# Performance work log

Hardware: AMD Instinct MI355X
Metric: run time of the kernel (lower is better)

The kernel has to match this reference:

```python
import jax, jax.numpy as jnp
import numpy as np

B = 1024      # batch of seed nodes
S = 16        # sample_size
H = 256       # hidden
IN = 150      # in_dim + NUM_CLASS (128 + 22)
OUT = 22
HEADS = 8
NN = 100000   # number of graph nodes
LN_EPS = 1e-5


def setup_inputs() -> dict:
    key = jax.random.key(0)
    ks = jax.random.split(key, 16)
    sc = 0.05
    return {
        "node_feats": jax.random.normal(ks[0], (NN, IN), jnp.float32),
        "batch": jax.random.randint(ks[1], (B,), 0, NN),
        "nbr2": jax.random.randint(ks[2], (B, S), 0, NN),
        "nbr1": jax.random.randint(ks[3], (B * (S + 1), S), 0, NN),
        "W_in": jax.random.normal(ks[4], (IN, H), jnp.float32) * sc,
        "b_in": jnp.zeros((H,), jnp.float32),
        "Wqkv": jax.random.normal(ks[5], (2, 3, H, H), jnp.float32) * sc,
        "bqkv": jnp.zeros((2, 3, H), jnp.float32),
        "Wo": jax.random.normal(ks[6], (2, H, H), jnp.float32) * sc,
        "bo": jnp.zeros((2, H), jnp.float32),
        "Wf": jax.random.normal(ks[7], (2, H, H), jnp.float32) * sc,
        "bf": jnp.zeros((2, H), jnp.float32),
        "ln_g": jnp.ones((4, H), jnp.float32),
        "ln_b": jnp.zeros((4, H), jnp.float32),
        "W_out": jax.random.normal(ks[8], (H, OUT), jnp.float32) * sc,
        "b_out": jnp.zeros((OUT,), jnp.float32),
    }


def _layer_norm(x, g, b):
    m = jnp.mean(x, axis=-1, keepdims=True)
    v = jnp.mean((x - m) ** 2, axis=-1, keepdims=True)
    return (x - m) * jax.lax.rsqrt(v + LN_EPS) * g + b


def _mha(q, kv, Wq, Wk, Wv, bq, bk, bv, Wout, bout):
    # q: [N, 1, H], kv: [N, S, H]; single-query multi-head attention
    N, Sk, _ = kv.shape
    dh = H // HEADS
    qp = (q @ Wq + bq).reshape(N, 1, HEADS, dh)
    kp = (kv @ Wk + bk).reshape(N, Sk, HEADS, dh)
    vp = (kv @ Wv + bv).reshape(N, Sk, HEADS, dh)
    att = jax.nn.softmax(
        jnp.einsum("nqhd,nkhd->nhqk", qp, kp) / np.float32(np.sqrt(dh)), axis=-1
    )
    o = jnp.einsum("nhqk,nkhd->nqhd", att, vp).reshape(N, 1, H)
    return o @ Wout + bout


def _attn_block(x, l, Wqkv, bqkv, Wo, bo, Wf, bf, ln_g, ln_b):
    # x: [N, S+1, H]; slot 0 is the query (self), rest are sampled neighbors
    q, kv = x[:, 0:1, :], x[:, 1:, :]
    h = _mha(q, kv, Wqkv[l, 0], Wqkv[l, 1], Wqkv[l, 2],
             bqkv[l, 0], bqkv[l, 1], bqkv[l, 2], Wo[l], bo[l])
    h = h[:, 0, :] + q[:, 0, :]                       # residual
    h = _layer_norm(h, ln_g[2 * l], ln_b[2 * l])
    h = h + (h @ Wf[l] + bf[l])                       # FFN (single Linear) + residual
    return _layer_norm(h, ln_g[2 * l + 1], ln_b[2 * l + 1])


def reference(node_feats, batch, nbr2, nbr1, W_in, b_in, Wqkv, bqkv, Wo, bo,
              Wf, bf, ln_g, ln_b, W_out, b_out):
    # Recursive neighbor expansion (unrolled for layers=2)
    ids1 = jnp.concatenate([batch[:, None], nbr2], axis=1).reshape(-1)   # [B*(S+1)]
    ids0 = jnp.concatenate([ids1[:, None], nbr1], axis=1).reshape(-1)    # [B*(S+1)^2]
    # layer 0: proj_in(features) = ReLU(Linear) (Dropout identity in eval)
    h0 = jax.nn.relu(node_feats[ids0] @ W_in + b_in)                     # [M0, H]
    # layer 1
    h1 = _attn_block(h0.reshape(B * (S + 1), S + 1, H), 0,
                     Wqkv, bqkv, Wo, bo, Wf, bf, ln_g, ln_b)
    # layer 2
    h2 = _attn_block(h1.reshape(B, S + 1, H), 1,
                     Wqkv, bqkv, Wo, bo, Wf, bf, ln_g, ln_b)
    # proj_out: Linear -> Softmax
    return jax.nn.softmax(h2 @ W_out + b_out, axis=-1)
```

## Files before the change

kernel.cpp:

```cpp
#include <hip/hip_runtime.h>
#include <hip/hip_bf16.h>
#include <math.h>

typedef unsigned short ushort_t;
typedef __bf16 bf16x8 __attribute__((ext_vector_type(8)));
typedef float  f32x4  __attribute__((ext_vector_type(4)));
typedef __attribute__((address_space(1))) const unsigned int* gas_t;
typedef __attribute__((address_space(3))) unsigned int* las_t;

#define B_SZ   1024
#define SEQ    17
#define KVN    16
#define HDIM   256
#define NHEAD  8
#define DH     32
#define INF    150
#define OUTD   22
#define LN_EPS 1e-5f
#define N1     (B_SZ * SEQ)
#define NN_    100000
#define NKVBLK 1563
#define NHQBLK 272

constexpr size_t SZ_H0    = (size_t)NN_ * 256 * 2;
constexpr size_t SZ_KV0   = (size_t)NN_ * 512 * 2;
constexpr size_t SZ_ROW   = (size_t)N1 * 256 * 2;
constexpr size_t OFF_HQ   = 0;
constexpr size_t OFF_KV0  = OFF_HQ + SZ_H0;
constexpr size_t OFF_QKV1 = OFF_KV0;
constexpr size_t OFF_O1   = OFF_QKV1 + (size_t)N1 * 768 * 2;
constexpr size_t OFF_H2   = OFF_O1 + (size_t)B_SZ * 256 * 2;
constexpr size_t OFF_Q0   = OFF_KV0 + SZ_KV0;
constexpr size_t OFF_O0   = OFF_Q0 + SZ_ROW;
constexpr size_t OFF_H1   = OFF_O0;
constexpr size_t OFF_IDS  = OFF_O0 + SZ_ROW;
constexpr size_t OFF_WTIN = OFF_IDS + (size_t)N1 * 4;
constexpr size_t OFF_WKV0 = OFF_WTIN + 256 * 160 * 2;
constexpr size_t OFF_WQ0  = OFF_WKV0 + 512 * 256 * 2;
constexpr size_t OFF_WKVQ1= OFF_WQ0 + 256 * 256 * 2;
constexpr size_t OFF_WO0  = OFF_WKVQ1 + 768 * 256 * 2;
constexpr size_t OFF_WF0  = OFF_WO0 + 256 * 256 * 2;
constexpr size_t OFF_WO1  = OFF_WF0 + 256 * 256 * 2;
constexpr size_t OFF_WF1  = OFF_WO1 + 256 * 256 * 2;
constexpr size_t OFF_B1   = OFF_WF1 + 256 * 256 * 2;

__device__ __forceinline__ ushort_t f2bfu(float x) {
    __hip_bfloat16 h = __float2bfloat16(x);
    return *reinterpret_cast<ushort_t*>(&h);
}
__device__ __forceinline__ float bfu2f(ushort_t u) {
    __hip_bfloat16 h;
    *reinterpret_cast<ushort_t*>(&h) = u;
    return __bfloat162float(h);
}
__device__ __forceinline__ f32x4 mfma16(bf16x8 a, bf16x8 b, f32x4 c) {
    return __builtin_amdgcn_mfma_f32_16x16x32_bf16(a, b, c, 0, 0, 0);
}

__device__ __forceinline__ void stage_b(
    const ushort_t* __restrict__ Bsrc, int Kld, int kk,
    ushort_t* lbase, int w, int lane) {
    #pragma unroll
    for (int i = 0; i < 4; ++i) {
        int inst = w * 4 + i;
        int row = inst * 16 + (lane >> 2);
        int q_log = (lane & 3) ^ ((row >> 1) & 3);
        const ushort_t* src = Bsrc + (size_t)row * Kld + kk + q_log * 8;
        __builtin_amdgcn_global_load_lds((gas_t)(const void*)src,
                                         (las_t)(void*)(lbase + inst * 512),
                                         16, 0, 0);
    }
}

__global__ __launch_bounds__(256) void k_prep(
    const float* __restrict__ W_in, const float* __restrict__ Wqkv,
    const float* __restrict__ Wo, const float* __restrict__ Wf,
    const float* __restrict__ bqkv,
    const int* __restrict__ batch, const int* __restrict__ nbr2,
    char* __restrict__ ws) {
    const int job = blockIdx.y;
    const int idx = blockIdx.x * 256 + threadIdx.x;
    if (job == 11) {
        if (idx < N1) {
            int b = idx / SEQ, s = idx % SEQ;
            ((int*)(ws + OFF_IDS))[idx] = (s == 0) ? batch[b] : nbr2[b * KVN + s - 1];
        }
        return;
    }
    if (job == 12) {
        if (idx < 768) ((float*)(ws + OFF_B1))[idx] = bqkv[768 + ((idx + 256) % 768)];
        return;
    }
    const float* src = nullptr; ushort_t* dst = nullptr;
    int Kpad = 256, Kvalid = 256;
    switch (job) {
        case 0:  src = W_in;           dst = (ushort_t*)(ws + OFF_WTIN); Kpad = 160; Kvalid = 150; break;
        case 1:  src = Wqkv + 65536;   dst = (ushort_t*)(ws + OFF_WKV0); break;
        case 2:  src = Wqkv + 131072;  dst = (ushort_t*)(ws + OFF_WKV0) + 65536; break;
        case 3:  src = Wqkv;           dst = (ushort_t*)(ws + OFF_WQ0); break;
        case 4:  src = Wqkv + 262144;  dst = (ushort_t*)(ws + OFF_WKVQ1); break;
        case 5:  src = Wqkv + 327680;  dst = (ushort_t*)(ws + OFF_WKVQ1) + 65536; break;
        case 6:  src = Wqkv + 196608;  dst = (ushort_t*)(ws + OFF_WKVQ1) + 131072; break;
        case 7:  src = Wo;             dst = (ushort_t*)(ws + OFF_WO0); break;
        case 8:  src = Wo + 65536;     dst = (ushort_t*)(ws + OFF_WO1); break;
        case 9:  src = Wf;             dst = (ushort_t*)(ws + OFF_WF0); break;
        case 10: src = Wf + 65536;     dst = (ushort_t*)(ws + OFF_WF1); break;
    }
    const int total = 256 * Kpad;
    if (idx >= total) return;
    int n = idx / Kpad, k = idx % Kpad;
    dst[idx] = (k < Kvalid) ? f2bfu(src[(size_t)k * 256 + n]) : (ushort_t)0;
}

__global__ __launch_bounds__(256) void k_fused(
    const float* __restrict__ nf,
    const ushort_t* __restrict__ Wt_in, const float* __restrict__ b_in,
    const ushort_t* __restrict__ Wkv, const ushort_t* __restrict__ Wq,
    const float* __restrict__ bqkv, const int* __restrict__ ids1,
    ushort_t* __restrict__ kv0, ushort_t* __restrict__ hq,
    ushort_t* __restrict__ q0) {
    __shared__ ushort_t Ah[64 * 256];
    __shared__ ushort_t Bbuf[2 * 8192];
    const int tid = threadIdx.x;
    const bool iskv = blockIdx.x < NKVBLK;
    const int m0 = (iskv ? blockIdx.x : blockIdx.x - NKVBLK) * 64;
    const int lane = tid & 63, w = tid >> 6;
    const int lr = lane & 15, q4 = lane >> 4, lk = q4 * 8;

    {
        ushort_t (*Astage)[168] = reinterpret_cast<ushort_t (*)[168]>(Ah);
        #pragma unroll
        for (int i = 0; i < 5; ++i) {
            int flat = tid + i * 256;
            int row = flat / 20, ch = flat % 20;
            int gm; 
            if (iskv) { gm = m0 + row; if (gm >= NN_) gm = 0; }
            else      { gm = ids1[m0 + row]; }
            const float* ap = nf + (size_t)gm * INF + ch * 8;
            ushort_t tmp[8];
            if (ch < 18) {
                #pragma unroll
                for (int j = 0; j < 4; ++j) {
                    float2 f = *reinterpret_cast<const float2*>(ap + j * 2);
                    tmp[j * 2] = f2bfu(f.x); tmp[j * 2 + 1] = f2bfu(f.y);
                }
            } else {
                #pragma unroll
                for (int j = 0; j < 8; ++j) {
                    int k = ch * 8 + j;
                    tmp[j] = (k < INF) ? f2bfu(ap[j]) : (ushort_t)0;
                }
            }
            *reinterpret_cast<int4*>(&Astage[row][ch * 8]) = *reinterpret_cast<int4*>(tmp);
        }
    }
    stage_b(Wt_in, 160, 0, Bbuf, w, lane);
    __syncthreads();

    f32x4 acc1[4][4] = {};
    {
        ushort_t (*Astage)[168] = reinterpret_cast<ushort_t (*)[168]>(Ah);
        for (int s = 0; s < 5; ++s) {
            const int cur = s & 1;
            if (s < 4) stage_b(Wt_in, 160, (s + 1) * 32, Bbuf + (cur ^ 1) * 8192, w, lane);
            bf16x8 a[4], b[4];
            #pragma unroll
            for (int mi = 0; mi < 4; ++mi)
                a[mi] = *reinterpret_cast<const bf16x8*>(&Astage[mi * 16 + lr][s * 32 + lk]);
            #pragma unroll
            for (int ni = 0; ni < 4; ++ni) {
                int n = w * 64 + ni * 16 + lr;
                b[ni] = *reinterpret_cast<const bf16x8*>(
                    &Bbuf[cur * 8192 + n * 32 + ((q4 ^ ((n >> 1) & 3)) * 8)]);
            }
            #pragma unroll
            for (int mi = 0; mi < 4; ++mi)
                #pragma unroll
                for (int ni = 0; ni < 4; ++ni)
                    acc1[mi][ni] = mfma16(a[mi], b[ni], acc1[mi][ni]);
            __syncthreads();
        }
    }

    #pragma unroll
    for (int ni = 0; ni < 4; ++ni) {
        int col = w * 64 + ni * 16 + lr;
        float bb = b_in[col];
        #pragma unroll
        for (int mi = 0; mi < 4; ++mi)
            #pragma unroll
            for (int r = 0; r < 4; ++r) {
                int row = mi * 16 + q4 * 4 + r;
                Ah[row * 256 + (col ^ ((row & 7) << 3))] =
                    f2bfu(fmaxf(acc1[mi][ni][r] + bb, 0.f));
            }
    }
    __syncthreads();

    if (!iskv) {
        #pragma unroll
        for (int i = 0; i < 8; ++i) {
            int flat = tid + i * 256;
            int row = flat >> 5, ch = flat & 31;
            *reinterpret_cast<int4*>(hq + (size_t)(m0 + row) * 256 + ch * 8) =
                *reinterpret_cast<const int4*>(&Ah[row * 256 + ((ch ^ (row & 7)) * 8)]);
        }
    }

    const int npass = iskv ? 2 : 1;
    for (int h = 0; h < npass; ++h) {
        const ushort_t* Bm = iskv ? (Wkv + (size_t)h * 65536) : Wq;
        const float* bias = iskv ? (bqkv + 256 + h * 256) : bqkv;
        __syncthreads();
        stage_b(Bm, 256, 0, Bbuf, w, lane);
        __syncthreads();
        f32x4 acc2[4][4] = {};
        for (int s = 0; s < 8; ++s) {
            const int cur = s & 1;
            if (s < 7) stage_b(Bm, 256, (s + 1) * 32, Bbuf + (cur ^ 1) * 8192, w, lane);
            bf16x8 a[4], b[4];
            #pragma unroll
            for (int mi = 0; mi < 4; ++mi) {
                int row = mi * 16 + lr;
                int chunk = (s * 4 + q4) ^ (row & 7);
                a[mi] = *reinterpret_cast<const bf16x8*>(&Ah[row * 256 + chunk * 8]);
            }
            #pragma unroll
            for (int ni = 0; ni < 4; ++ni) {
                int n = w * 64 + ni * 16 + lr;
                b[ni] = *reinterpret_cast<const bf16x8*>(
                    &Bbuf[cur * 8192 + n * 32 + ((q4 ^ ((n >> 1) & 3)) * 8)]);
            }
            #pragma unroll
            for (int mi = 0; mi < 4; ++mi)
                #pragma unroll
                for (int ni = 0; ni < 4; ++ni)
                    acc2[mi][ni] = mfma16(a[mi], b[ni], acc2[mi][ni]);
            __syncthreads();
        }
        float bl[4];
        #pragma unroll
        for (int ni = 0; ni < 4; ++ni) bl[ni] = bias[w * 64 + ni * 16 + lr];
        ushort_t* outp = iskv ? kv0 : q0;
        const int ldo = iskv ? 512 : 256;
        const int coff = (iskv ? h * 256 : 0) + w * 64;
        ushort_t* Shw = Bbuf + w * 32 * 72;
        #pragma unroll
        for (int part = 0; part < 2; ++part) {
            #pragma unroll
            for (int mi2 = 0; mi2 < 2; ++mi2) {
                int mi = part * 2 + mi2;
                #pragma unroll
                for (int ni = 0; ni < 4; ++ni)
                    #pragma unroll
                    for (int r = 0; r < 4; ++r)
                        Shw[(mi2 * 16 + q4 * 4 + r) * 72 + ni * 16 + lr] =
                            f2bfu(acc2[mi][ni][r] + bl[ni]);
            }
            #pragma unroll
            for (int j = 0; j < 4; ++j) {
                int flat = lane + j * 64;
                int r32 = flat >> 3, ch = flat & 7;
                int grow = m0 + part * 32 + r32;
                if (!iskv || grow < NN_)
                    *reinterpret_cast<int4*>(outp + (size_t)grow * ldo + coff + ch * 8) =
                        *reinterpret_cast<const int4*>(&Shw[r32 * 72 + ch * 8]);
            }
        }
    }
}

__global__ __launch_bounds__(256) void k_ffn(
    const ushort_t* __restrict__ Ain, const ushort_t* __restrict__ W1t,
    const float* __restrict__ b1,
    const ushort_t* __restrict__ resmat, int rstride,
    const float* __restrict__ lng1, const float* __restrict__ lnb1,
    const ushort_t* __restrict__ W2t, const float* __restrict__ b2,
    const float* __restrict__ lng2, const float* __restrict__ lnb2,
    ushort_t* __restrict__ out) {
    __shared__ ushort_t Al[32][264];
    __shared__ float xr[32][260];
    __shared__ float mrow[32], rrow[32];
    const int tid = threadIdx.x;
    const int m0 = blockIdx.x * 32;
    const int lane = tid & 63, w = tid >> 6;
    const int lr = lane & 15, q4 = lane >> 4, lk = q4 * 8;

    #pragma unroll
    for (int j = 0; j < 4; ++j) {
        int flat = tid + j * 256;
        int row = flat >> 5, ch = flat & 31;
        *reinterpret_cast<int4*>(&Al[row][ch * 8]) =
            *reinterpret_cast<const int4*>(Ain + (size_t)(m0 + row) * 256 + ch * 8);
    }
    __syncthreads();

    f32x4 acc[2][4];
    #pragma unroll
    for (int g = 0; g < 2; ++g) {
        const ushort_t* Wt = g ? W2t : W1t;
        #pragma unroll
        for (int mi = 0; mi < 2; ++mi)
            #pragma unroll
            for (int ni = 0; ni < 4; ++ni) acc[mi][ni] = f32x4{0.f, 0.f, 0.f, 0.f};
        bf16x8 bc[4];
        #pragma unroll
        for (int ni = 0; ni < 4; ++ni)
            bc[ni] = *reinterpret_cast<const bf16x8*>(
                Wt + (size_t)(w * 64 + ni * 16 + lr) * 256 + lk);
        #pragma unroll
        for (int s = 0; s < 8; ++s) {
            bf16x8 bn[4];
            if (s < 7) {
                #pragma unroll
                for (int ni = 0; ni < 4; ++ni)
                    bn[ni] = *reinterpret_cast<const bf16x8*>(
                        Wt + (size_t)(w * 64 + ni * 16 + lr) * 256 + (s + 1) * 32 + lk);
            }
            bf16x8 a0 = *reinterpret_cast<const bf16x8*>(&Al[lr][s * 32 + lk]);
            bf16x8 a1 = *reinterpret_cast<const bf16x8*>(&Al[16 + lr][s * 32 + lk]);
            #pragma unroll
            for (int ni = 0; ni < 4; ++ni) {
                acc[0][ni] = mfma16(a0, bc[ni], acc[0][ni]);
                acc[1][ni] = mfma16(a1, bc[ni], acc[1][ni]);
            }
            if (s < 7) {
                #pragma unroll
                for (int ni = 0; ni < 4; ++ni) bc[ni] = bn[ni];
            }
        }
        #pragma unroll
        for (int mi = 0; mi < 2; ++mi)
            #pragma unroll
            for (int ni = 0; ni < 4; ++ni)
                #pragma unroll
                for (int r = 0; r < 4; ++r)
                    xr[mi * 16 + q4 * 4 + r][w * 64 + ni * 16 + lr] = acc[mi][ni][r];
        __syncthreads();
        {
            float bb = g ? b2[tid] : b1[tid];
            if (g == 0) {
                for (int r = 0; r < 32; ++r)
                    xr[r][tid] += bb + bfu2f(resmat[(size_t)(m0 + r) * rstride * 256 + tid]);
            } else {
                for (int r = 0; r < 32; ++r)
                    xr[r][tid] += bb + bfu2f(Al[r][tid]);
            }
        }
        __syncthreads();
        for (int rr = w * 8; rr < w * 8 + 8; ++rr) {
            float4 v = *reinterpret_cast<const float4*>(&xr[rr][lane * 4]);
            float s1 = v.x + v.y + v.z + v.w;
            float s2 = v.x * v.x + v.y * v.y + v.z * v.z + v.w * v.w;
            #pragma unroll
            for (int off = 32; off > 0; off >>= 1) {
                s1 += __shfl_xor(s1, off);
                s2 += __shfl_xor(s2, off);
            }
            if (lane == 0) {
                float m = s1 * (1.f / 256.f);
                float var = s2 * (1.f / 256.f) - m * m;
                mrow[rr] = m;
                rrow[rr] = rsqrtf(var + LN_EPS);
            }
        }
        __syncthreads();
        if (g == 0) {
            float gg = lng1[tid], bb = lnb1[tid];
            for (int r = 0; r < 32; ++r)
                Al[r][tid] = f2bfu((xr[r][tid] - mrow[r]) * rrow[r] * gg + bb);
        } else {
            float gg = lng2[tid], bb = lnb2[tid];
            for (int r = 0; r < 32; ++r)
                out[(size_t)(m0 + r) * 256 + tid] =
                    f2bfu((xr[r][tid] - mrow[r]) * rrow[r] * gg + bb);
        }
        __syncthreads();
    }
}

__global__ __launch_bounds__(256) void k_qkv1(
    const ushort_t* __restrict__ h1, const ushort_t* __restrict__ Wt,
    const float* __restrict__ bias, ushort_t* __restrict__ outm) {
    __shared__ ushort_t Ah[64 * 256];
    __shared__ ushort_t Sh[4][32][72];
    const int tid = threadIdx.x;
    const int m0 = blockIdx.x * 64;
    const int lane = tid & 63, w = tid >> 6;
    const int lr = lane & 15, q4 = lane >> 4, lk = q4 * 8;

    #pragma unroll
    for (int i = 0; i < 8; ++i) {
        int flat = tid + i * 256;
        int row = flat >> 5, ch = flat & 31;
        *reinterpret_cast<int4*>(&Ah[row * 256 + ((ch ^ (row & 7)) * 8)]) =
            *reinterpret_cast<const int4*>(h1 + (size_t)(m0 + row) * 256 + ch * 8);
    }
    __syncthreads();

    for (int p = 0; p < 3; ++p) {
        f32x4 acc[4][4] = {};
        bf16x8 bc[4];
        #pragma unroll
        for (int ni = 0; ni < 4; ++ni)
            bc[ni] = *reinterpret_cast<const bf16x8*>(
                Wt + (size_t)(p * 256 + w * 64 + ni * 16 + lr) * 256 + lk);
        #pragma unroll
        for (int s = 0; s < 8; ++s) {
            bf16x8 bn[4];
            if (s < 7) {
                #pragma unroll
                for (int ni = 0; ni < 4; ++ni)
                    bn[ni] = *reinterpret_cast<const bf16x8*>(
                        Wt + (size_t)(p * 256 + w * 64 + ni * 16 + lr) * 256 + (s + 1) * 32 + lk);
            }
            bf16x8 a[4];
            #pragma unroll
            for (int mi = 0; mi < 4; ++mi) {
                int row = mi * 16 + lr;
                int chunk = (s * 4 + q4) ^ (row & 7);
                a[mi] = *reinterpret_cast<const bf16x8*>(&Ah[row * 256 + chunk * 8]);
            }
            #pragma unroll
            for (int mi = 0; mi < 4; ++mi)
                #pragma unroll
                for (int ni = 0; ni < 4; ++ni)
                    acc[mi][ni] = mfma16(a[mi], bc[ni], acc[mi][ni]);
            if (s < 7) {
                #pragma unroll
                for (int ni = 0; ni < 4; ++ni) bc[ni] = bn[ni];
            }
        }
        float bl[4];
        #pragma unroll
        for (int ni = 0; ni < 4; ++ni) bl[ni] = bias[p * 256 + w * 64 + ni * 16 + lr];
        const int coff = p * 256 + w * 64;
        #pragma unroll
        for (int part = 0; part < 2; ++part) {
            #pragma unroll
            for (int mi2 = 0; mi2 < 2; ++mi2) {
                int mi = part * 2 + mi2;
                #pragma unroll
                for (int ni = 0; ni < 4; ++ni)
                    #pragma unroll
                    for (int r = 0; r < 4; ++r)
                        Sh[w][mi2 * 16 + q4 * 4 + r][ni * 16 + lr] =
                            f2bfu(acc[mi][ni][r] + bl[ni]);
            }
            #pragma unroll
            for (int j = 0; j < 4; ++j) {
                int flat = lane + j * 64;
                int r32 = flat >> 3, ch = flat & 7;
                int grow = m0 + part * 32 + r32;
                *reinterpret_cast<int4*>(outm + (size_t)grow * 768 + coff + ch * 8) =
                    *reinterpret_cast<const int4*>(&Sh[w][r32][ch * 8]);
            }
        }
    }
}

__global__ __launch_bounds__(256) void attn_wave(
    const ushort_t* __restrict__ q_all, int qld, int qoff, int qstride,
    const ushort_t* __restrict__ kv_all, int kvld, int koff, int voff,
    const int* __restrict__ kvidx, int ngroups, ushort_t* __restrict__ o_out) {
    __shared__ ushort_t KL[4][KVN][264];
    __shared__ ushort_t VL[4][KVN][264];
    const int w = threadIdx.x >> 6, lane = threadIdx.x & 63;
    const int g = blockIdx.x * 4 + w;
    if (g >= ngroups) return;

    int idx16 = 0;
    if (lane < KVN)
        idx16 = kvidx ? kvidx[g * KVN + lane] : g * SEQ + 1 + lane;

    float qv[4];
    {
        uint2 u = *reinterpret_cast<const uint2*>(
            q_all + (size_t)g * qstride * qld + qoff + lane * 4);
        qv[0] = bfu2f((ushort_t)(u.x & 0xffff));
        qv[1] = bfu2f((ushort_t)(u.x >> 16));
        qv[2] = bfu2f((ushort_t)(u.y & 0xffff));
        qv[3] = bfu2f((ushort_t)(u.y >> 16));
    }
    {
        const int r = lane & 15, qtr = lane >> 4;
        int rid = __shfl(idx16, r);
        const ushort_t* kb = kv_all + (size_t)rid * kvld + koff;
        const ushort_t* vb = kv_all + (size_t)rid * kvld + voff;
        #pragma unroll
        for (int j = 0; j < 8; ++j) {
            int c8 = (qtr * 8 + j) * 8;
            *reinterpret_cast<int4*>(&KL[w][r][c8]) = *reinterpret_cast<const int4*>(kb + c8);
            *reinterpret_cast<int4*>(&VL[w][r][c8]) = *reinterpret_cast<const int4*>(vb + c8);
        }
    }
    float att[KVN];
    #pragma unroll
    for (int k = 0; k < KVN; ++k) {
        uint2 u = *reinterpret_cast<const uint2*>(&KL[w][k][lane * 4]);
        float p = qv[0] * bfu2f((ushort_t)(u.x & 0xffff))
                + qv[1] * bfu2f((ushort_t)(u.x >> 16))
                + qv[2] * bfu2f((ushort_t)(u.y & 0xffff))
                + qv[3] * bfu2f((ushort_t)(u.y >> 16));
        p += __shfl_xor(p, 1);
        p += __shfl_xor(p, 2);
        p += __shfl_xor(p, 4);
        att[k] = p * 0.17677669529663687f;
    }
    float m = att[0];
    #pragma unroll
    for (int k = 1; k < KVN; ++k) m = fmaxf(m, att[k]);
    float sum = 0.f;
    #pragma unroll
    for (int k = 0; k < KVN; ++k) { att[k] = __expf(att[k] - m); sum += att[k]; }
    float inv = 1.f / sum;
    float o[4] = {0.f, 0.f, 0.f, 0.f};
    #pragma unroll
    for (int k = 0; k < KVN; ++k) {
        uint2 u = *reinterpret_cast<const uint2*>(&VL[w][k][lane * 4]);
        float a = att[k] * inv;
        o[0] += a * bfu2f((ushort_t)(u.x & 0xffff));
        o[1] += a * bfu2f((ushort_t)(u.x >> 16));
        o[2] += a * bfu2f((ushort_t)(u.y & 0xffff));
        o[3] += a * bfu2f((ushort_t)(u.y >> 16));
    }
    uint2 r;
    r.x = (unsigned)f2bfu(o[0]) | ((unsigned)f2bfu(o[1]) << 16);
    r.y = (unsigned)f2bfu(o[2]) | ((unsigned)f2bfu(o[3]) << 16);
    *reinterpret_cast<uint2*>(o_out + (size_t)g * 256 + lane * 4) = r;
}

__global__ __launch_bounds__(64) void k_out(
    const ushort_t* __restrict__ h2, const float* __restrict__ W_out,
    const float* __restrict__ b_out, float* __restrict__ out) {
    const int b = blockIdx.x, j = threadIdx.x;
    __shared__ float xr[HDIM];
    for (int k = j; k < HDIM; k += 64) xr[k] = bfu2f(h2[(size_t)b * HDIM + k]);
    __syncthreads();
    float logit = -1e30f;
    if (j < OUTD) {
        float acc = b_out[j];
        for (int k = 0; k < HDIM; ++k) acc += xr[k] * W_out[k * OUTD + j];
        logit = acc;
    }
    float m = logit;
    #pragma unroll
    for (int off = 32; off > 0; off >>= 1) m = fmaxf(m, __shfl_xor(m, off));
    float e = (j < OUTD) ? __expf(logit - m) : 0.f;
    float s = e;
    #pragma unroll
    for (int off = 32; off > 0; off >>= 1) s += __shfl_xor(s, off);
    if (j < OUTD) out[(size_t)b * OUTD + j] = e / s;
}

extern "C" void kernel_launch(void* const* d_in, const int* in_sizes, int n_in,
                              void* d_out, int out_size, void* d_ws, size_t ws_size,
                              hipStream_t stream) {
    const float* nf    = (const float*)d_in[0];
    const int*   batch = (const int*)d_in[1];
    const int*   nbr2  = (const int*)d_in[2];
    const int*   nbr1  = (const int*)d_in[3];
    const float* W_in  = (const float*)d_in[4];
    const float* b_in  = (const float*)d_in[5];
    const float* Wqkv  = (const float*)d_in[6];
    const float* bqkv  = (const float*)d_in[7];
    const float* Wo    = (const float*)d_in[8];
    const float* bo    = (const float*)d_in[9];
    const float* Wf    = (const float*)d_in[10];
    const float* bf    = (const float*)d_in[11];
    const float* ln_g  = (const float*)d_in[12];
    const float* ln_b  = (const float*)d_in[13];
    const float* W_out = (const float*)d_in[14];
    const float* b_out = (const float*)d_in[15];
    float* out = (float*)d_out;
    char* ws = (char*)d_ws;

    ushort_t* hq   = (ushort_t*)(ws + OFF_HQ);
    ushort_t* kv0  = (ushort_t*)(ws + OFF_KV0);
    ushort_t* q0   = (ushort_t*)(ws + OFF_Q0);
    ushort_t* o0   = (ushort_t*)(ws + OFF_O0);
    ushort_t* h1   = (ushort_t*)(ws + OFF_H1);
    ushort_t* qkv1 = (ushort_t*)(ws + OFF_QKV1);
    ushort_t* o1   = (ushort_t*)(ws + OFF_O1);
    ushort_t* h2   = (ushort_t*)(ws + OFF_H2);
    const int* ids1 = (const int*)(ws + OFF_IDS);

    hipLaunchKernelGGL(k_prep, dim3(256, 13), dim3(256), 0, stream,
                       W_in, Wqkv, Wo, Wf, bqkv, batch, nbr2, ws);
    hipLaunchKernelGGL(k_fused, dim3(NKVBLK + NHQBLK), dim3(256), 0, stream,
                       nf, (const ushort_t*)(ws + OFF_WTIN), b_in,
                       (const ushort_t*)(ws + OFF_WKV0),
                       (const ushort_t*)(ws + OFF_WQ0), bqkv, ids1,
                       kv0, hq, q0);
    hipLaunchKernelGGL(attn_wave, dim3(N1 / 4), dim3(256), 0, stream,
                       q0, 256, 0, 1, kv0, 512, 0, 256, nbr1, N1, o0);
    hipLaunchKernelGGL(k_ffn, dim3(N1 / 32), dim3(256), 0, stream,
                       o0, (const ushort_t*)(ws + OFF_WO0), bo,
                       hq, 1, ln_g, ln_b,
                       (const ushort_t*)(ws + OFF_WF0), bf,
                       ln_g + 256, ln_b + 256, h1);
    hipLaunchKernelGGL(k_qkv1, dim3(N1 / 64), dim3(256), 0, stream,
                       h1, (const ushort_t*)(ws + OFF_WKVQ1),
                       (const float*)(ws + OFF_B1), qkv1);
    hipLaunchKernelGGL(attn_wave, dim3(B_SZ / 4), dim3(256), 0, stream,
                       qkv1, 768, 512, 17, qkv1, 768, 0, 256,
                       (const int*)nullptr, B_SZ, o1);
    hipLaunchKernelGGL(k_ffn, dim3(B_SZ / 32), dim3(256), 0, stream,
                       o1, (const ushort_t*)(ws + OFF_WO1), bo + 256,
                       h1, 17, ln_g + 512, ln_b + 512,
                       (const ushort_t*)(ws + OFF_WF1), bf + 256,
                       ln_g + 768, ln_b + 768, h2);
    hipLaunchKernelGGL(k_out, dim3(B_SZ), dim3(64), 0, stream,
                       h2, W_out, b_out, out);
}
```

Before: 275.8 us.

## Enlarge fused projection tile to 128 rows with 512-thread blocks

The fused input-projection and KV/Q-projection kernel now processes 128 rows per block with 8 waves in a 2x4 grid instead of 64 rows with 4 waves. Each staged weight tile is reused across twice as many rows, which halves weight traffic per output row. Double-buffered weight staging is replaced by a single buffer with barriers around each stage, so load latency is no longer hidden behind compute. The epilogue drops the LDS-staged coalesced 16-byte stores and writes scalar bf16 values straight to global memory, which may cost store efficiency. Shared memory per block grows to about 80KB, which limits how many blocks fit on a CU.

After: 306.6 us. +11.2%, slower.

```diff
diff --git a/kernel.cpp b/kernel.cpp
--- a/kernel.cpp
+++ b/kernel.cpp
@@ -19,8 +19,8 @@
 #define LN_EPS 1e-5f
 #define N1     (B_SZ * SEQ)
 #define NN_    100000
-#define NKVBLK 1563
-#define NHQBLK 272
+#define NKV2   782
+#define NHQ2   136
 
 constexpr size_t SZ_H0    = (size_t)NN_ * 256 * 2;
 constexpr size_t SZ_KV0   = (size_t)NN_ * 512 * 2;
@@ -57,12 +57,12 @@
     return __builtin_amdgcn_mfma_f32_16x16x32_bf16(a, b, c, 0, 0, 0);
 }
 
-__device__ __forceinline__ void stage_b(
+__device__ __forceinline__ void stage_b512(
     const ushort_t* __restrict__ Bsrc, int Kld, int kk,
     ushort_t* lbase, int w, int lane) {
     #pragma unroll
-    for (int i = 0; i < 4; ++i) {
-        int inst = w * 4 + i;
+    for (int i = 0; i < 2; ++i) {
+        int inst = w * 2 + i;
         int row = inst * 16 + (lane >> 2);
         int q_log = (lane & 3) ^ ((row >> 1) & 3);
         const ushort_t* src = Bsrc + (size_t)row * Kld + kk + q_log * 8;
@@ -112,28 +112,29 @@
     dst[idx] = (k < Kvalid) ? f2bfu(src[(size_t)k * 256 + n]) : (ushort_t)0;
 }
 
-__global__ __launch_bounds__(256) void k_fused(
+__global__ __launch_bounds__(512, 4) void k_fused(
     const float* __restrict__ nf,
     const ushort_t* __restrict__ Wt_in, const float* __restrict__ b_in,
     const ushort_t* __restrict__ Wkv, const ushort_t* __restrict__ Wq,
     const float* __restrict__ bqkv, const int* __restrict__ ids1,
     ushort_t* __restrict__ kv0, ushort_t* __restrict__ hq,
     ushort_t* __restrict__ q0) {
-    __shared__ ushort_t Ah[64 * 256];
-    __shared__ ushort_t Bbuf[2 * 8192];
+    __shared__ ushort_t Ah[128 * 256];
+    __shared__ ushort_t Bst[8192];
     const int tid = threadIdx.x;
-    const bool iskv = blockIdx.x < NKVBLK;
-    const int m0 = (iskv ? blockIdx.x : blockIdx.x - NKVBLK) * 64;
+    const bool iskv = blockIdx.x < NKV2;
+    const int m0 = (iskv ? blockIdx.x : blockIdx.x - NKV2) * 128;
     const int lane = tid & 63, w = tid >> 6;
+    const int wr = w >> 2, wc = w & 3;
     const int lr = lane & 15, q4 = lane >> 4, lk = q4 * 8;
 
     {
         ushort_t (*Astage)[168] = reinterpret_cast<ushort_t (*)[168]>(Ah);
         #pragma unroll
         for (int i = 0; i < 5; ++i) {
-            int flat = tid + i * 256;
+            int flat = tid + i * 512;
             int row = flat / 20, ch = flat % 20;
-            int gm; 
+            int gm;
             if (iskv) { gm = m0 + row; if (gm >= NN_) gm = 0; }
             else      { gm = ids1[m0 + row]; }
             const float* ap = nf + (size_t)gm * INF + ch * 8;
@@ -154,43 +155,44 @@
             *reinterpret_cast<int4*>(&Astage[row][ch * 8]) = *reinterpret_cast<int4*>(tmp);
         }
     }
-    stage_b(Wt_in, 160, 0, Bbuf, w, lane);
     __syncthreads();
 
     f32x4 acc1[4][4] = {};
     {
         ushort_t (*Astage)[168] = reinterpret_cast<ushort_t (*)[168]>(Ah);
         for (int s = 0; s < 5; ++s) {
-            const int cur = s & 1;
-            if (s < 4) stage_b(Wt_in, 160, (s + 1) * 32, Bbuf + (cur ^ 1) * 8192, w, lane);
+            __builtin_amdgcn_s_barrier();
+            stage_b512(Wt_in, 160, s * 32, Bst, w, lane);
+            __syncthreads();
             bf16x8 a[4], b[4];
             #pragma unroll
             for (int mi = 0; mi < 4; ++mi)
-                a[mi] = *reinterpret_cast<const bf16x8*>(&Astage[mi * 16 + lr][s * 32 + lk]);
+                a[mi] = *reinterpret_cast<const bf16x8*>(
+                    &Astage[wr * 64 + mi * 16 + lr][s * 32 + lk]);
             #pragma unroll
             for (int ni = 0; ni < 4; ++ni) {
-                int n = w * 64 + ni * 16 + lr;
+                int n = wc * 64 + ni * 16 + lr;
                 b[ni] = *reinterpret_cast<const bf16x8*>(
-                    &Bbuf[cur * 8192 + n * 32 + ((q4 ^ ((n >> 1) & 3)) * 8)]);
+                    &Bst[n * 32 + ((q4 ^ ((n >> 1) & 3)) * 8)]);
             }
             #pragma unroll
             for (int mi = 0; mi < 4; ++mi)
                 #pragma unroll
                 for (int ni = 0; ni < 4; ++ni)
                     acc1[mi][ni] = mfma16(a[mi], b[ni], acc1[mi][ni]);
-            __syncthreads();
-        }
-    }
+        }
+    }
+    __syncthreads();
 
     #pragma unroll
     for (int ni = 0; ni < 4; ++ni) {
-        int col = w * 64 + ni * 16 + lr;
+        int col = wc * 64 + ni * 16 + lr;
         float bb = b_in[col];
         #pragma unroll
         for (int mi = 0; mi < 4; ++mi)
             #pragma unroll
             for (int r = 0; r < 4; ++r) {
-                int row = mi * 16 + q4 * 4 + r;
+                int row = wr * 64 + mi * 16 + q4 * 4 + r;
                 Ah[row * 256 + (col ^ ((row & 7) << 3))] =
                     f2bfu(fmaxf(acc1[mi][ni][r] + bb, 0.f));
             }
@@ -200,7 +202,7 @@
     if (!iskv) {
         #pragma unroll
         for (int i = 0; i < 8; ++i) {
-            int flat = tid + i * 256;
+            int flat = tid + i * 512;
             int row = flat >> 5, ch = flat & 31;
             *reinterpret_cast<int4*>(hq + (size_t)(m0 + row) * 256 + ch * 8) =
                 *reinterpret_cast<const int4*>(&Ah[row * 256 + ((ch ^ (row & 7)) * 8)]);
@@ -211,61 +213,45 @@
     for (int h = 0; h < npass; ++h) {
         const ushort_t* Bm = iskv ? (Wkv + (size_t)h * 65536) : Wq;
         const float* bias = iskv ? (bqkv + 256 + h * 256) : bqkv;
-        __syncthreads();
-        stage_b(Bm, 256, 0, Bbuf, w, lane);
-        __syncthreads();
         f32x4 acc2[4][4] = {};
         for (int s = 0; s < 8; ++s) {
-            const int cur = s & 1;
-            if (s < 7) stage_b(Bm, 256, (s + 1) * 32, Bbuf + (cur ^ 1) * 8192, w, lane);
+            __builtin_amdgcn_s_barrier();
+            stage_b512(Bm, 256, s * 32, Bst, w, lane);
+            __syncthreads();
             bf16x8 a[4], b[4];
             #pragma unroll
             for (int mi = 0; mi < 4; ++mi) {
-                int row = mi * 16 + lr;
+                int row = wr * 64 + mi * 16 + lr;
                 int chunk = (s * 4 + q4) ^ (row & 7);
                 a[mi] = *reinterpret_cast<const bf16x8*>(&Ah[row * 256 + chunk * 8]);
             }
             #pragma unroll
             for (int ni = 0; ni < 4; ++ni) {
-                int n = w * 64 + ni * 16 + lr;
+                int n = wc * 64 + ni * 16 + lr;
                 b[ni] = *reinterpret_cast<const bf16x8*>(
-                    &Bbuf[cur * 8192 + n * 32 + ((q4 ^ ((n >> 1) & 3)) * 8)]);
+                    &Bst[n * 32 + ((q4 ^ ((n >> 1) & 3)) * 8)]);
             }
             #pragma unroll
             for (int mi = 0; mi < 4; ++mi)
                 #pragma unroll
                 for (int ni = 0; ni < 4; ++ni)
                     acc2[mi][ni] = mfma16(a[mi], b[ni], acc2[mi][ni]);
-            __syncthreads();
-        }
-        float bl[4];
-        #pragma unroll
-        for (int ni = 0; ni < 4; ++ni) bl[ni] = bias[w * 64 + ni * 16 + lr];
+        }
         ushort_t* outp = iskv ? kv0 : q0;
         const int ldo = iskv ? 512 : 256;
-        const int coff = (iskv ? h * 256 : 0) + w * 64;
-        ushort_t* Shw = Bbuf + w * 32 * 72;
-        #pragma unroll
-        for (int part = 0; part < 2; ++part) {
-            #pragma unroll
-            for (int mi2 = 0; mi2 < 2; ++mi2) {
-                int mi = part * 2 + mi2;
-                #pragma unroll
-                for (int ni = 0; ni < 4; ++ni)
-                    #pragma unroll
-                    for (int r = 0; r < 4; ++r)
-                        Shw[(mi2 * 16 + q4 * 4 + r) * 72 + ni * 16 + lr] =
-                            f2bfu(acc2[mi][ni][r] + bl[ni]);
-            }
-            #pragma unroll
-            for (int j = 0; j < 4; ++j) {
-                int flat = lane + j * 64;
-                int r32 = flat >> 3, ch = flat & 7;
-                int grow = m0 + part * 32 + r32;
-                if (!iskv || grow < NN_)
-                    *reinterpret_cast<int4*>(outp + (size_t)grow * ldo + coff + ch * 8) =
-                        *reinterpret_cast<const int4*>(&Shw[r32 * 72 + ch * 8]);
-            }
+        const int coff = (iskv ? h * 256 : 0) + wc * 64;
+        #pragma unroll
+        for (int ni = 0; ni < 4; ++ni) {
+            float bb = bias[wc * 64 + ni * 16 + lr];
+            #pragma unroll
+            for (int mi = 0; mi < 4; ++mi)
+                #pragma unroll
+                for (int r = 0; r < 4; ++r) {
+                    int grow = m0 + wr * 64 + mi * 16 + q4 * 4 + r;
+                    if (!iskv || grow < NN_)
+                        outp[(size_t)grow * ldo + coff + ni * 16 + lr] =
+                            f2bfu(acc2[mi][ni][r] + bb);
+                }
         }
     }
 }
@@ -587,7 +573,7 @@
 
     hipLaunchKernelGGL(k_prep, dim3(256, 13), dim3(256), 0, stream,
                        W_in, Wqkv, Wo, Wf, bqkv, batch, nbr2, ws);
-    hipLaunchKernelGGL(k_fused, dim3(NKVBLK + NHQBLK), dim3(256), 0, stream,
+    hipLaunchKernelGGL(k_fused, dim3(NKV2 + NHQ2), dim3(512), 0, stream,
                        nf, (const ushort_t*)(ws + OFF_WTIN), b_in,
                        (const ushort_t*)(ws + OFF_WKV0),
                        (const ushort_t*)(ws + OFF_WQ0), bqkv, ids1,
```
